# Kernel optimization log

Hardware: AMD Instinct MI355X
Metric: run time of the kernel (lower is better)

## Reference

```python
import jax, jax.numpy as jnp
import numpy as np

NUM_HEADS = 8


def _attn(q, k, v, scale):
    # q: [B,H,Nq,d], k/v: [B,H,Nk,d]
    a = jax.nn.softmax(jnp.einsum('bhqd,bhkd->bhqk', q, k) * scale, axis=-1)
    return jnp.einsum('bhqk,bhkd->bhqd', a, v)


def setup_inputs() -> dict:
    key = jax.random.key(0)
    k1, k2, k3 = jax.random.split(key, 3)
    B, N, C = 8, 1024, 768
    x = jax.random.normal(k1, (B, N, C), dtype=jnp.float32)
    w_qkv = jax.random.normal(k2, (3 * C, C), dtype=jnp.float32) * 0.02
    w_proj = jax.random.normal(k3, (C, C), dtype=jnp.float32) * 0.02
    b_proj = jnp.zeros((C,), dtype=jnp.float32)
    return {"x": x, "w_qkv": w_qkv, "w_proj": w_proj, "b_proj": b_proj}


def reference(x, w_qkv, w_proj, b_proj):
    B, N, C = x.shape
    H = NUM_HEADS
    hd = C // H            # full head dim (scale uses this, per the source)
    g = hd // 3            # per-group head dim
    scale = hd ** (-0.5)

    qkv = (x @ w_qkv.T).reshape(B, N, 3, H, hd).transpose(2, 0, 3, 1, 4)  # [3,B,H,N,hd]
    q, k, v = qkv[0], qkv[1], qkv[2]

    q3, q4, q5 = q[..., :g], q[..., g:2 * g], q[..., 2 * g:]
    k3, k4, k5 = k[..., :g], k[..., g:2 * g], k[..., 2 * g:]
    v3, v4, v5 = v[..., :g], v[..., g:2 * g], v[..., 2 * g:]

    def merge(o):  # [B,H,N,g] -> [B,N,H*g]
        return o.transpose(0, 2, 1, 3).reshape(B, N, C // 3)

    x3 = merge(_attn(q4, jnp.concatenate([k3, k4], axis=2), jnp.concatenate([v3, v4], axis=2), scale))
    x4 = merge(_attn(q5, jnp.concatenate([k3, k5], axis=2), jnp.concatenate([v3, v5], axis=2), scale))
    x5 = merge(_attn(q5, jnp.concatenate([k4, k5], axis=2), jnp.concatenate([v4, v5], axis=2), scale))

    out = jnp.concatenate([x3, x4, x5], axis=2)
    return out @ w_proj.T + b_proj
```

## Files before the change

### kernel.cpp

```cpp
#include <hip/hip_runtime.h>
#include <hip/hip_bf16.h>

typedef unsigned short u16;
typedef __attribute__((ext_vector_type(8))) short short8;
typedef __attribute__((ext_vector_type(4))) float f32x4;

__device__ __forceinline__ u16 f2b(float f) {
  union { float f; unsigned u; } a; a.f = f;
  unsigned r = a.u + 0x7fffu + ((a.u >> 16) & 1u);
  return (u16)(r >> 16);
}

__device__ __forceinline__ unsigned pkbf16(float lo, float hi) {
  unsigned r;
  asm("v_cvt_pk_bf16_f32 %0, %1, %2" : "=v"(r) : "v"(lo), "v"(hi));
  return r;
}

#define GLD_LDS16(gp, lp) __builtin_amdgcn_global_load_lds( \
    (const __attribute__((address_space(1))) void*)(gp),    \
    (__attribute__((address_space(3))) void*)(lp), 16, 0, 0)

__global__ __launch_bounds__(256) void cvt3(
    const float* __restrict__ x, const float* __restrict__ wq, const float* __restrict__ wp,
    u16* __restrict__ xb, u16* __restrict__ wqb, u16* __restrict__ wpb)
{
  const int NX = 8192 * 768 / 4, NQ = 2304 * 768 / 4, NP = 768 * 768 / 4;
  int i = blockIdx.x * 256 + threadIdx.x;
  const float* src; u16* dst; int j;
  float sc = 1.0f;
  if (i < NX)            { src = x;  dst = xb;  j = i; }
  else if (i < NX + NQ)  { src = wq; dst = wqb; j = i - NX;
                           if (j < 147456) sc = 0.14724447f; }
  else if (i < NX + NQ + NP) { src = wp; dst = wpb; j = i - NX - NQ; }
  else return;
  float4 v = *(const float4*)&src[(size_t)j * 4];
  u16 o[4] = { f2b(v.x * sc), f2b(v.y * sc), f2b(v.z * sc), f2b(v.w * sc) };
  *(uint2*)&dst[(size_t)j * 4] = *(uint2*)o;
}

__global__ __launch_bounds__(256) void gemm_bt(
    const u16* __restrict__ A, const u16* __restrict__ Bt,
    u16* __restrict__ Cb, float* __restrict__ Cf, const float* __restrict__ bias,
    int M, int N, int K)
{
  __shared__ u16 Al[128 * 32];
  __shared__ u16 Bl[128 * 32];
  const int tid = threadIdx.x;
  const int lane = tid & 63, wave = tid >> 6;
  const int wr = wave >> 1, wc = wave & 1;
  const int g = lane >> 4, c16 = lane & 15;
  const int m0 = blockIdx.y * 128, n0 = blockIdx.x * 128;

  f32x4 acc[4][4] = {};

  const int c0 = tid, c1 = tid + 256;
  const int r0 = c0 >> 2, o0 = (c0 & 3) * 8;
  const int r1 = c1 >> 2, o1 = (c1 & 3) * 8;
  const u16* a0 = A + (size_t)(m0 + r0) * K + o0;
  const u16* a1 = A + (size_t)(m0 + r1) * K + o1;
  const u16* b0 = Bt + (size_t)(n0 + r0) * K + o0;
  const u16* b1 = Bt + (size_t)(n0 + r1) * K + o1;

  for (int k0 = 0; k0 < K; k0 += 32) {
    GLD_LDS16(a0 + k0, Al + c0 * 8);
    GLD_LDS16(a1 + k0, Al + c1 * 8);
    GLD_LDS16(b0 + k0, Bl + c0 * 8);
    GLD_LDS16(b1 + k0, Bl + c1 * 8);
    __syncthreads();
    short8 af[4], bfr[4];
#pragma unroll
    for (int m = 0; m < 4; ++m)
      af[m] = *(const short8*)&Al[(wr * 64 + m * 16 + c16) * 32 + g * 8];
#pragma unroll
    for (int n = 0; n < 4; ++n)
      bfr[n] = *(const short8*)&Bl[(wc * 64 + n * 16 + c16) * 32 + g * 8];
#pragma unroll
    for (int m = 0; m < 4; ++m)
#pragma unroll
      for (int n = 0; n < 4; ++n)
        acc[m][n] = __builtin_amdgcn_mfma_f32_16x16x32_bf16(af[m], bfr[n], acc[m][n], 0, 0, 0);
    __syncthreads();
  }

  if (Cb) {
#pragma unroll
    for (int m = 0; m < 4; ++m) {
      const int row = m0 + wr * 64 + m * 16 + g * 4;
#pragma unroll
      for (int n = 0; n < 4; ++n) {
        const int col = n0 + wc * 64 + n * 16 + c16;
#pragma unroll
        for (int j = 0; j < 4; ++j)
          Cb[(size_t)(row + j) * N + col] = f2b(acc[m][n][j]);
      }
    }
  } else {
#pragma unroll
    for (int m = 0; m < 4; ++m) {
      const int row = m0 + wr * 64 + m * 16 + g * 4;
#pragma unroll
      for (int n = 0; n < 4; ++n) {
        const int col = n0 + wc * 64 + n * 16 + c16;
        const float bb = bias[col];
#pragma unroll
        for (int j = 0; j < 4; ++j)
          Cf[(size_t)(row + j) * N + col] = acc[m][n][j] + bb;
      }
    }
  }
}

__global__ __launch_bounds__(256) void vtrans(const u16* __restrict__ qkv, u16* __restrict__ vt)
{
  __shared__ u16 Vtl[96 * 72];
  const int tid = threadIdx.x;
  const int bh = blockIdx.x >> 4, nt = blockIdx.x & 15;
  const int b = bh >> 3, h = bh & 7;
  const int n0 = nt * 64;
  const size_t tb = (size_t)b * 1024;
#pragma unroll
  for (int i = 0; i < 3; ++i) {
    int c = tid + i * 256;
    int key = c / 12, cc = c % 12;
    uint4 v = *(const uint4*)&qkv[(tb + n0 + key) * 2304 + 1536 + h * 96 + cc * 8];
    union { uint4 u; u16 s[8]; } cv; cv.u = v;
#pragma unroll
    for (int j = 0; j < 8; ++j)
      Vtl[(cc * 8 + j) * 72 + key] = cv.s[j];
  }
  __syncthreads();
#pragma unroll
  for (int i = 0; i < 3; ++i) {
    int c = tid + i * 256;
    int d = c >> 3, c2 = c & 7;
    int chunk = c2 >> 2;
    int kA = ((c2 & 1) << 4) | ((c2 & 2) << 1);
    const u16* src = &Vtl[d * 72 + c2 * 8];
    size_t base = ((size_t)bh * 96 + d) * 1024 + n0 + chunk * 32;
    *(uint2*)&vt[base + kA]     = *(const uint2*)(src);
    *(uint2*)&vt[base + kA + 8] = *(const uint2*)(src + 4);
  }
}

__global__ __launch_bounds__(256, 3) void attn_kernel(
    const u16* __restrict__ qkv, const u16* __restrict__ vt, u16* __restrict__ feat)
{
  __shared__ u16 Kl[3][64 * 40];
  __shared__ u16 Vl[96 * 72];

  const int tid = threadIdx.x;
  const int lane = tid & 63;
  const int g = lane >> 4, c16 = lane & 15;
  const int id = blockIdx.x;
  const int h = id & 7, qt = (id >> 3) & 15, b = id >> 7;
  const int bh = b * 8 + h;
  const int q0 = qt * 64 + (tid >> 6) * 16;
  const size_t tb = (size_t)b * 1024;

  short8 qf[2];
#pragma unroll
  for (int qs = 0; qs < 2; ++qs)
    qf[qs] = *(const short8*)&qkv[(tb + q0 + c16) * 2304 + h * 96 + 32 + 32 * qs + 8 * g];

  short8 ones;
#pragma unroll
  for (int i = 0; i < 8; ++i) ones[i] = (short)0x3F80;

  f32x4 acc[4][2] = {};
  f32x4 lsv[4] = {};

  int kk_key[3], kk_cc[3], vv_d[3], vv_c[3];
#pragma unroll
  for (int i = 0; i < 3; ++i) {
    int c = tid + i * 256;
    kk_key[i] = c / 12; kk_cc[i] = c % 12;
    vv_d[i] = c >> 3;   vv_c[i] = c & 7;
  }
  uint4 kst[3], vst[3];
#pragma unroll
  for (int i = 0; i < 3; ++i) {
    kst[i] = *(const uint4*)&qkv[(tb + kk_key[i]) * 2304 + 768 + h * 96 + kk_cc[i] * 8];
    vst[i] = *(const uint4*)&vt[((size_t)bh * 96 + vv_d[i]) * 1024 + vv_c[i] * 8];
  }

  const int ATT[5] = {0, 0, 1, 3, 2};
  const int QS[5]  = {0, 0, 1, 1, 1};
  const int KS[5]  = {0, 1, 0, 2, 1};

  for (int t = 0; t < 16; ++t) {
    __syncthreads();
#pragma unroll
    for (int i = 0; i < 3; ++i) {
      int part = kk_cc[i] >> 2, g4 = kk_cc[i] & 3;
      *(uint4*)&Kl[part][kk_key[i] * 40 + g4 * 8] = kst[i];
      *(uint4*)&Vl[vv_d[i] * 72 + vv_c[i] * 8] = vst[i];
    }
    if (t < 15) {
      int kv0 = (t + 1) * 64;
#pragma unroll
      for (int i = 0; i < 3; ++i) {
        kst[i] = *(const uint4*)&qkv[(tb + kv0 + kk_key[i]) * 2304 + 768 + h * 96 + kk_cc[i] * 8];
        vst[i] = *(const uint4*)&vt[((size_t)bh * 96 + vv_d[i]) * 1024 + kv0 + vv_c[i] * 8];
      }
    }
    __syncthreads();

#pragma unroll
    for (int u = 0; u < 5; ++u) {
      const int att = ATT[u], qs = QS[u], ks = KS[u];
      short8 kf[4], vf[2][2];
#pragma unroll
      for (int n = 0; n < 4; ++n)
        kf[n] = *(const short8*)&Kl[ks][(n * 16 + c16) * 40 + g * 8];
#pragma unroll
      for (int n = 0; n < 2; ++n)
#pragma unroll
        for (int kk = 0; kk < 2; ++kk)
          vf[n][kk] = *(const short8*)&Vl[(ks * 32 + n * 16 + c16) * 72 + kk * 32 + g * 8];

      const f32x4 z = {0.f, 0.f, 0.f, 0.f};
      f32x4 St[4];
      __builtin_amdgcn_s_setprio(1);
#pragma unroll
      for (int n = 0; n < 4; ++n)
        St[n] = __builtin_amdgcn_mfma_f32_16x16x32_bf16(kf[n], qf[qs], z, 0, 0, 0);
      __builtin_amdgcn_s_setprio(0);
      short8 pa[2];
#pragma unroll
      for (int kk = 0; kk < 2; ++kk) {
        union { unsigned u[4]; short8 s; } w;
        w.u[0] = pkbf16(__builtin_amdgcn_exp2f(St[2 * kk][0]),     __builtin_amdgcn_exp2f(St[2 * kk][1]));
        w.u[1] = pkbf16(__builtin_amdgcn_exp2f(St[2 * kk][2]),     __builtin_amdgcn_exp2f(St[2 * kk][3]));
        w.u[2] = pkbf16(__builtin_amdgcn_exp2f(St[2 * kk + 1][0]), __builtin_amdgcn_exp2f(St[2 * kk + 1][1]));
        w.u[3] = pkbf16(__builtin_amdgcn_exp2f(St[2 * kk + 1][2]), __builtin_amdgcn_exp2f(St[2 * kk + 1][3]));
        pa[kk] = w.s;
      }
      __builtin_amdgcn_s_setprio(1);
#pragma unroll
      for (int n = 0; n < 2; ++n)
#pragma unroll
        for (int kk = 0; kk < 2; ++kk)
          acc[att][n] = __builtin_amdgcn_mfma_f32_16x16x32_bf16(pa[kk], vf[n][kk], acc[att][n], 0, 0, 0);
#pragma unroll
      for (int kk = 0; kk < 2; ++kk)
        lsv[att] = __builtin_amdgcn_mfma_f32_16x16x32_bf16(pa[kk], ones, lsv[att], 0, 0, 0);
      __builtin_amdgcn_s_setprio(0);
    }
  }

  lsv[1] += lsv[3];
  lsv[2] += lsv[3];
#pragma unroll
  for (int n = 0; n < 2; ++n) {
    acc[1][n] += acc[3][n];
    acc[2][n] += acc[3][n];
  }

#pragma unroll
  for (int a = 0; a < 3; ++a) {
    f32x4 inv;
#pragma unroll
    for (int r = 0; r < 4; ++r) inv[r] = 1.0f / lsv[a][r];
#pragma unroll
    for (int n = 0; n < 2; ++n)
#pragma unroll
      for (int r = 0; r < 4; ++r) {
        int row = q0 + g * 4 + r;
        int col = a * 256 + h * 32 + n * 16 + c16;
        feat[(tb + row) * 768 + col] = f2b(acc[a][n][r] * inv[r]);
      }
  }
}

extern "C" void kernel_launch(void* const* d_in, const int* in_sizes, int n_in,
                              void* d_out, int out_size, void* d_ws, size_t ws_size,
                              hipStream_t stream) {
  const float* x  = (const float*)d_in[0];
  const float* wq = (const float*)d_in[1];
  const float* wp = (const float*)d_in[2];
  const float* bp = (const float*)d_in[3];
  float* out = (float*)d_out;

  char* ws = (char*)d_ws;
  u16* xb    = (u16*)(ws);
  u16* wqb   = (u16*)(ws + 12582912);
  u16* wpb   = (u16*)(ws + 16121856);
  u16* qkvb  = (u16*)(ws + 17301504);
  u16* vtb   = (u16*)(ws + 55050240);
  u16* featb = xb;

  cvt3<<<8448, 256, 0, stream>>>(x, wq, wp, xb, wqb, wpb);
  gemm_bt<<<dim3(18, 64), 256, 0, stream>>>(xb, wqb, qkvb, nullptr, nullptr, 8192, 2304, 768);
  vtrans<<<1024, 256, 0, stream>>>(qkvb, vtb);
  attn_kernel<<<1024, 256, 0, stream>>>(qkvb, vtb, featb);
  gemm_bt<<<dim3(6, 64), 256, 0, stream>>>(featb, wpb, nullptr, out, bp, 8192, 768, 768);
}
```

Before: 206.1 us.

## Stage attention output through LDS for coalesced stores and permute proj weights

The attention epilogue now writes normalized outputs into per-wave LDS tiles and then emits 16-byte coalesced stores into a head-contiguous feature layout, replacing scattered 2-byte global stores. To keep the math consistent, the projection weight conversion permutes its input columns to match the new feature ordering. V fragment loads are moved after the QK MFMAs, and the launch-bounds occupancy hint drops from 3 to 2 blocks, which may relieve register pressure but could lower occupancy.

```diff
diff --git a/kernel.cpp b/kernel.cpp
--- a/kernel.cpp
+++ b/kernel.cpp
@@ -27,16 +27,24 @@
 {
   const int NX = 8192 * 768 / 4, NQ = 2304 * 768 / 4, NP = 768 * 768 / 4;
   int i = blockIdx.x * 256 + threadIdx.x;
-  const float* src; u16* dst; int j;
-  float sc = 1.0f;
-  if (i < NX)            { src = x;  dst = xb;  j = i; }
-  else if (i < NX + NQ)  { src = wq; dst = wqb; j = i - NX;
-                           if (j < 147456) sc = 0.14724447f; }
-  else if (i < NX + NQ + NP) { src = wp; dst = wpb; j = i - NX - NQ; }
-  else return;
-  float4 v = *(const float4*)&src[(size_t)j * 4];
-  u16 o[4] = { f2b(v.x * sc), f2b(v.y * sc), f2b(v.z * sc), f2b(v.w * sc) };
-  *(uint2*)&dst[(size_t)j * 4] = *(uint2*)o;
+  if (i < NX) {
+    float4 v = *(const float4*)&x[(size_t)i * 4];
+    u16 o[4] = { f2b(v.x), f2b(v.y), f2b(v.z), f2b(v.w) };
+    *(uint2*)&xb[(size_t)i * 4] = *(uint2*)o;
+  } else if (i < NX + NQ) {
+    int j = i - NX;
+    float sc = (j < 147456) ? 0.14724447f : 1.0f;
+    float4 v = *(const float4*)&wq[(size_t)j * 4];
+    u16 o[4] = { f2b(v.x * sc), f2b(v.y * sc), f2b(v.z * sc), f2b(v.w * sc) };
+    *(uint2*)&wqb[(size_t)j * 4] = *(uint2*)o;
+  } else if (i < NX + NQ + NP) {
+    int j = i - NX - NQ;
+    int oo = (j * 4) / 768, ii = (j * 4) % 768;
+    int a = ii >> 8, h = (ii >> 5) & 7, c = ii & 31;
+    float4 v = *(const float4*)&wp[(size_t)j * 4];
+    u16 o[4] = { f2b(v.x), f2b(v.y), f2b(v.z), f2b(v.w) };
+    *(uint2*)&wpb[oo * 768 + h * 96 + a * 32 + c] = *(uint2*)o;
+  }
 }
 
 __global__ __launch_bounds__(256) void gemm_bt(
@@ -143,19 +151,20 @@
   }
 }
 
-__global__ __launch_bounds__(256, 3) void attn_kernel(
+__global__ __launch_bounds__(256, 2) void attn_kernel(
     const u16* __restrict__ qkv, const u16* __restrict__ vt, u16* __restrict__ feat)
 {
-  __shared__ u16 Kl[3][64 * 40];
-  __shared__ u16 Vl[96 * 72];
+  __shared__ u16 smem[3 * 64 * 40 + 96 * 72];
+  u16* Kl = smem;
+  u16* Vl = smem + 3 * 64 * 40;
 
   const int tid = threadIdx.x;
-  const int lane = tid & 63;
+  const int lane = tid & 63, wave = tid >> 6;
   const int g = lane >> 4, c16 = lane & 15;
   const int id = blockIdx.x;
   const int h = id & 7, qt = (id >> 3) & 15, b = id >> 7;
   const int bh = b * 8 + h;
-  const int q0 = qt * 64 + (tid >> 6) * 16;
+  const int q0 = qt * 64 + wave * 16;
   const size_t tb = (size_t)b * 1024;
 
   short8 qf[2];
@@ -193,7 +202,7 @@
 #pragma unroll
     for (int i = 0; i < 3; ++i) {
       int part = kk_cc[i] >> 2, g4 = kk_cc[i] & 3;
-      *(uint4*)&Kl[part][kk_key[i] * 40 + g4 * 8] = kst[i];
+      *(uint4*)&Kl[part * 2560 + kk_key[i] * 40 + g4 * 8] = kst[i];
       *(uint4*)&Vl[vv_d[i] * 72 + vv_c[i] * 8] = vst[i];
     }
     if (t < 15) {
@@ -209,15 +218,10 @@
 #pragma unroll
     for (int u = 0; u < 5; ++u) {
       const int att = ATT[u], qs = QS[u], ks = KS[u];
-      short8 kf[4], vf[2][2];
+      short8 kf[4];
 #pragma unroll
       for (int n = 0; n < 4; ++n)
-        kf[n] = *(const short8*)&Kl[ks][(n * 16 + c16) * 40 + g * 8];
-#pragma unroll
-      for (int n = 0; n < 2; ++n)
-#pragma unroll
-        for (int kk = 0; kk < 2; ++kk)
-          vf[n][kk] = *(const short8*)&Vl[(ks * 32 + n * 16 + c16) * 72 + kk * 32 + g * 8];
+        kf[n] = *(const short8*)&Kl[ks * 2560 + (n * 16 + c16) * 40 + g * 8];
 
       const f32x4 z = {0.f, 0.f, 0.f, 0.f};
       f32x4 St[4];
@@ -226,6 +230,12 @@
       for (int n = 0; n < 4; ++n)
         St[n] = __builtin_amdgcn_mfma_f32_16x16x32_bf16(kf[n], qf[qs], z, 0, 0, 0);
       __builtin_amdgcn_s_setprio(0);
+      short8 vf[2][2];
+#pragma unroll
+      for (int n = 0; n < 2; ++n)
+#pragma unroll
+        for (int kk = 0; kk < 2; ++kk)
+          vf[n][kk] = *(const short8*)&Vl[(ks * 32 + n * 16 + c16) * 72 + kk * 32 + g * 8];
       short8 pa[2];
 #pragma unroll
       for (int kk = 0; kk < 2; ++kk) {
@@ -257,6 +267,8 @@
     acc[2][n] += acc[3][n];
   }
 
+  __syncthreads();
+  u16* Ol = smem + wave * 1536;
 #pragma unroll
   for (int a = 0; a < 3; ++a) {
     f32x4 inv;
@@ -265,11 +277,15 @@
 #pragma unroll
     for (int n = 0; n < 2; ++n)
 #pragma unroll
-      for (int r = 0; r < 4; ++r) {
-        int row = q0 + g * 4 + r;
-        int col = a * 256 + h * 32 + n * 16 + c16;
-        feat[(tb + row) * 768 + col] = f2b(acc[a][n][r] * inv[r]);
-      }
+      for (int r = 0; r < 4; ++r)
+        Ol[(g * 4 + r) * 96 + a * 32 + n * 16 + c16] = f2b(acc[a][n][r] * inv[r]);
+  }
+#pragma unroll
+  for (int i = 0; i < 3; ++i) {
+    int chunk = lane + 64 * i;
+    int row = chunk / 12, cc = chunk % 12;
+    uint4 val = *(const uint4*)&Ol[row * 96 + cc * 8];
+    *(uint4*)&feat[(tb + q0 + row) * 768 + h * 96 + cc * 8] = val;
   }
 }
 
```

Result: no change. 206.6 us (+0.2%).
